# Kernel tuning notes

Hardware: AMD Instinct MI355X
Metric: run time of the kernel (lower is better)

Reference implementation:

```python
import jax, jax.numpy as jnp
import numpy as np

B, T, F, H = 64, 1024, 160, 1024


def setup_inputs() -> dict:
    key = jax.random.key(0)
    ks = jax.random.split(key, 18)
    s = lambda k, shape, scale=0.05: (jax.random.normal(k, shape, jnp.float32) * scale)
    inp = {
        "x": jax.random.normal(ks[0], (B, T, F), jnp.float32),
        # encoder GRU layer 0 (input F -> hidden H), PyTorch gate order r,z,n
        "Wih0": s(ks[1], (3 * H, F)), "Whh0": s(ks[2], (3 * H, H)),
        "bih0": s(ks[3], (3 * H,)), "bhh0": s(ks[4], (3 * H,)),
        # encoder GRU layer 1 (input H -> hidden H)
        "Wih1": s(ks[5], (3 * H, H)), "Whh1": s(ks[6], (3 * H, H)),
        "bih1": s(ks[7], (3 * H,)), "bhh1": s(ks[8], (3 * H,)),
        # fc: (n_enc_layers*H) -> H
        "fcW": s(ks[9], (H, 2 * H)), "fcb": jnp.zeros((H,), jnp.float32),
        # decoder GRUCell (input F -> hidden H)
        "dWih": s(ks[10], (3 * H, F)), "dWhh": s(ks[11], (3 * H, H)),
        "dbih": s(ks[12], (3 * H,)), "dbhh": s(ks[13], (3 * H,)),
        # dec_proj: H -> F
        "pW": s(ks[14], (F, H)), "pb": jnp.zeros((F,), jnp.float32),
    }
    return inp


def gru_step(h, xt, Wih, Whh, bih, bhh):
    # PyTorch GRU/GRUCell math, gate order (r, z, n)
    gi = xt @ Wih.T + bih          # [B, 3H]
    gh = h @ Whh.T + bhh           # [B, 3H]
    ir, iz, inn = jnp.split(gi, 3, axis=-1)
    hr, hz, hn = jnp.split(gh, 3, axis=-1)
    r = jax.nn.sigmoid(ir + hr)
    z = jax.nn.sigmoid(iz + hz)
    n = jnp.tanh(inn + r * hn)
    return (1.0 - z) * n + z * h


def reference(x, Wih0, Whh0, bih0, bhh0, Wih1, Whh1, bih1, bhh1,
              fcW, fcb, dWih, dWhh, dbih, dbhh, pW, pb):
    Bx, Tx = x.shape[0], x.shape[1]
    xs = jnp.swapaxes(x, 0, 1)  # [T, B, F]

    def run_layer(seq, Wih, Whh, bih, bhh):
        h0 = jnp.zeros((Bx, Whh.shape[1]), x.dtype)
        def step(h, xt):
            h = gru_step(h, xt, Wih, Whh, bih, bhh)
            return h, h
        hT, hs = jax.lax.scan(step, h0, seq)
        return hT, hs

    # 2-layer encoder GRU (dropout disabled: eval-mode / deterministic reference)
    h1, hs0 = run_layer(xs, Wih0, Whh0, bih0, bhh0)
    h2, _ = run_layer(hs0, Wih1, Whh1, bih1, bhh1)

    # h_n permute+view -> concat(layer0, layer1) along features
    h = jnp.tanh(jnp.concatenate([h1, h2], axis=-1) @ fcW.T + fcb)  # [B, H]

    i0 = jnp.zeros((Bx, pW.shape[0]), x.dtype)
    def dec_step(carry, _):
        hd, i = carry
        hd = gru_step(hd, i, dWih, dWhh, dbih, dbhh)
        i = hd @ pW.T + pb
        return (hd, i), i
    _, outs = jax.lax.scan(dec_step, (h, i0), None, length=Tx)  # [T, B, F]
    return jnp.swapaxes(outs, 0, 1)  # [B, T, F]
```

## Files before the change

### kernel.cpp

```cpp
#include <hip/hip_runtime.h>
#include <math.h>

#define NWG 256
#define NTH 512
#define MASTER 255

typedef _Float16 f16;
typedef __attribute__((ext_vector_type(8))) _Float16 h8;
typedef __attribute__((ext_vector_type(4))) float f4;

namespace {
constexpr int T_ = 1024, F_ = 160, H_ = 1024;
constexpr float SC = 2048.f;
constexpr float INV = 1.f / 2048.f;

constexpr int ESLOTH = 512 * 64 * 8;
constexpr int DSLOTH = 256 * 64 * 8;
constexpr int ELO = 256;
constexpr int DLO = 128;

constexpr size_t WS_BAR  = 0;
constexpr size_t WS_CVEC = 32896;
constexpr size_t WS_WDEC = WS_CVEC + 12288;
constexpr size_t WS_ENCA = WS_WDEC + (size_t)4 * H_ * H_ * 4;
constexpr size_t WS_DECA = WS_ENCA + (size_t)2 * ESLOTH * 2;
constexpr size_t WS_STRM = WS_DECA + (size_t)2 * DSLOTH * 2;

constexpr int DBUF_B = 135168;
constexpr int TBUF_B = DBUF_B + 17408;
constexpr int ZP_B   = TBUF_B + 2048;
constexpr int LDS_B  = ZP_B + 64;
}

__device__ __forceinline__ f4 MF(h8 a, h8 b, f4 c) {
  return __builtin_amdgcn_mfma_f32_16x16x32_f16(a, b, c, 0, 0, 0);
}

__device__ __forceinline__ void fsplit(float v, f16& hi, f16& lo) {
  const float hf = (fabsf(v) >= 6.103515625e-05f) ? (float)(f16)v : 0.f;
  hi = (f16)hf;
  lo = (f16)((v - hf) * SC);
}

__device__ __forceinline__ void gbar(unsigned* bar, int wg, unsigned& phase) {
  __syncthreads();
  ++phase;
  const int tid = threadIdx.x;
  unsigned* gen = bar + 8192;
  if (wg == MASTER) {
    if (tid == 0)
      __hip_atomic_store(&bar[MASTER * 32], phase, __ATOMIC_RELEASE, __HIP_MEMORY_SCOPE_AGENT);
    if (tid < 256) {
      while (__hip_atomic_load(&bar[tid * 32], __ATOMIC_RELAXED, __HIP_MEMORY_SCOPE_AGENT) < phase)
        __builtin_amdgcn_s_sleep(1);
    }
    __syncthreads();
    if (tid == 0) {
      __hip_atomic_store(gen, phase, __ATOMIC_RELEASE, __HIP_MEMORY_SCOPE_AGENT);
      (void)__hip_atomic_load(gen, __ATOMIC_ACQUIRE, __HIP_MEMORY_SCOPE_AGENT);
    }
  } else {
    if (tid == 0) {
      __hip_atomic_store(&bar[wg * 32], phase, __ATOMIC_RELEASE, __HIP_MEMORY_SCOPE_AGENT);
      while (__hip_atomic_load(gen, __ATOMIC_RELAXED, __HIP_MEMORY_SCOPE_AGENT) < phase)
        __builtin_amdgcn_s_sleep(1);
      (void)__hip_atomic_load(gen, __ATOMIC_ACQUIRE, __HIP_MEMORY_SCOPE_AGENT);
    }
  }
  __syncthreads();
}

__device__ void stageEnc(f16* __restrict__ whi, f16* __restrict__ wlo,
                         const float* __restrict__ Wx, const float* __restrict__ Wh,
                         int KX, int XOo, int KO, int u0, int tid) {
  for (int task = tid; task < KO * 24; task += NTH) {
    const int oct = task / 24;
    const int sl = task - oct * 24;
    const int g = (sl < 16) ? (sl >> 3) : 2;
    const int u = u0 + (sl & 7);
    const float* src = (oct < XOo)
        ? (Wx + (size_t)(g * H_ + u) * KX + (size_t)oct * 8)
        : (Wh + (size_t)(g * H_ + u) * H_ + (size_t)(oct - XOo) * 8);
    const float4 a = *(const float4*)src;
    const float4 b = *(const float4*)(src + 4);
    const float v[8] = {a.x, a.y, a.z, a.w, b.x, b.y, b.z, b.w};
    h8 hv, lv;
#pragma unroll
    for (int e = 0; e < 8; ++e) { f16 hh, ll; fsplit(v[e], hh, ll); hv[e] = hh; lv[e] = ll; }
    *(h8*)(whi + ((size_t)oct * 25 + sl) * 8) = hv;
    if (wlo) *(h8*)(wlo + ((size_t)oct * 25 + sl) * 8) = lv;
  }
}

__device__ void stageDec(f16* __restrict__ whi, f16* __restrict__ wlo,
                         const float* __restrict__ wdec, const float* __restrict__ dWhh,
                         int u0, int tid, bool t1set) {
  for (int task = tid; task < 128 * 32; task += NTH) {
    const int oct = task >> 5, sl = task & 31;
    const int g = sl >> 3;
    const int u = u0 + (sl & 7);
    float v[8];
    if (t1set) {
      if (g == 2) {
#pragma unroll
        for (int e = 0; e < 8; ++e) v[e] = 0.f;
      } else {
        const float* s = dWhh + (size_t)((g == 3 ? 2 : g) * H_ + u) * H_ + (size_t)oct * 8;
        const float4 a = *(const float4*)s, b = *(const float4*)(s + 4);
        v[0]=a.x; v[1]=a.y; v[2]=a.z; v[3]=a.w; v[4]=b.x; v[5]=b.y; v[6]=b.z; v[7]=b.w;
      }
    } else {
      const float* s = wdec + (size_t)(g * H_ + u) * H_ + (size_t)oct * 8;
      const float4 a = *(const float4*)s, b = *(const float4*)(s + 4);
      v[0]=a.x; v[1]=a.y; v[2]=a.z; v[3]=a.w; v[4]=b.x; v[5]=b.y; v[6]=b.z; v[7]=b.w;
    }
    h8 hv, lv;
#pragma unroll
    for (int e = 0; e < 8; ++e) { f16 hh, ll; fsplit(v[e], hh, ll); hv[e] = hh; lv[e] = ll; }
    *(h8*)(whi + ((size_t)oct * 33 + sl) * 8) = hv;
    *(h8*)(wlo + ((size_t)oct * 33 + sl) * 8) = lv;
  }
}

__device__ void stageProj(f16* __restrict__ whi, f16* __restrict__ wlo,
                          const float* __restrict__ pW, int f0, int tid) {
  for (int task = tid; task < 128 * 16; task += NTH) {
    const int oct = task >> 4, sl = task & 15;
    const float* s = pW + (size_t)(f0 + sl) * H_ + (size_t)oct * 8;
    const float4 a = *(const float4*)s, b = *(const float4*)(s + 4);
    const float v[8] = {a.x, a.y, a.z, a.w, b.x, b.y, b.z, b.w};
    h8 hv, lv;
#pragma unroll
    for (int e = 0; e < 8; ++e) { f16 hh, ll; fsplit(v[e], hh, ll); hv[e] = hh; lv[e] = ll; }
    *(h8*)(whi + ((size_t)oct * 17 + sl) * 8) = hv;
    *(h8*)(wlo + ((size_t)oct * 17 + sl) * 8) = lv;
  }
}

template<int NT, bool NSPLIT, int ROWH, bool STRM>
__device__ __forceinline__ void gmm(f4* Dh, f4* Dc,
    const f16* __restrict__ Ab, int aoctBase, int loOct,
    const f16* __restrict__ whi, const f16* __restrict__ wlo,
    const f16* __restrict__ strm,
    int ktn, int octBase, int XO, int ls, int lq, int lane,
    const f16* __restrict__ zp) {
  auto LD = [&](int kk, h8& ah, h8& al, h8& bh0, h8& bl0, h8& bh1, h8& bl1) {
    const int aoct = aoctBase + kk * 4 + lq;
    ah = *(const h8*)(Ab + (size_t)aoct * 512);
    al = *(const h8*)(Ab + (size_t)(aoct + loOct) * 512);
    const int oct = octBase + kk * 4 + lq;
    bh0 = *(const h8*)(whi + ((size_t)oct * ROWH + ls) * 8);
    if constexpr (STRM) bl0 = *(const h8*)(strm + ((size_t)(kk * 2) * 64 + lane) * 8);
    else bl0 = *(const h8*)(wlo + ((size_t)oct * ROWH + ls) * 8);
    if constexpr (NT == 2) {
      bool act = true; int psl;
      if constexpr (NSPLIT) { act = (ls < 8) ? (oct < XO) : (oct >= XO); psl = 16 + (ls & 7); }
      else { psl = 16 + ls; }
      bh1 = *(const h8*)(act ? (whi + ((size_t)oct * ROWH + psl) * 8) : zp);
      if constexpr (STRM) bl1 = *(const h8*)(strm + ((size_t)(kk * 2 + 1) * 64 + lane) * 8);
      else bl1 = *(const h8*)(act ? (wlo + ((size_t)oct * ROWH + psl) * 8) : zp);
    }
  };
  h8 ah, al, bh0, bl0, bh1, bl1;
  LD(0, ah, al, bh0, bl0, bh1, bl1);
  for (int kk = 0; kk < ktn; ++kk) {
    h8 ah2, al2, bh02, bl02, bh12, bl12;
    const int nk = (kk + 1 < ktn) ? (kk + 1) : kk;
    LD(nk, ah2, al2, bh02, bl02, bh12, bl12);
    Dh[0] = MF(ah, bh0, Dh[0]);
    Dc[0] = MF(al, bh0, Dc[0]);
    Dc[0] = MF(ah, bl0, Dc[0]);
    if constexpr (NT == 2) {
      Dh[1] = MF(ah, bh1, Dh[1]);
      Dc[1] = MF(al, bh1, Dc[1]);
      Dc[1] = MF(ah, bl1, Dc[1]);
    }
    ah = ah2; al = al2; bh0 = bh02; bl0 = bl02;
    if constexpr (NT == 2) { bh1 = bh12; bl1 = bl12; }
  }
}

__device__ __forceinline__ void gmm_x(f4* Dh, f4* Dc, const float* __restrict__ xp,
    const f16* __restrict__ whi, const f16* __restrict__ wlo,
    int ls, int lq, const f16* __restrict__ zp) {
#pragma unroll
  for (int kk = 0; kk < 5; ++kk) {
    const float4 a = *(const float4*)(xp + kk * 32);
    const float4 b = *(const float4*)(xp + kk * 32 + 4);
    const float v[8] = {a.x, a.y, a.z, a.w, b.x, b.y, b.z, b.w};
    h8 ah, al;
#pragma unroll
    for (int e = 0; e < 8; ++e) { f16 hh, ll; fsplit(v[e], hh, ll); ah[e] = hh; al[e] = ll; }
    const int oct = kk * 4 + lq;
    {
      const h8 bh2 = *(const h8*)(whi + ((size_t)oct * 25 + ls) * 8);
      const h8 bl2 = *(const h8*)(wlo + ((size_t)oct * 25 + ls) * 8);
      Dh[0] = MF(ah, bh2, Dh[0]);
      Dc[0] = MF(al, bh2, Dc[0]);
      Dc[0] = MF(ah, bl2, Dc[0]);
    }
    {
      const bool act = (ls < 8);
      const int psl = 16 + (ls & 7);
      const h8 bh2 = *(const h8*)(act ? (whi + ((size_t)oct * 25 + psl) * 8) : zp);
      const h8 bl2 = *(const h8*)(act ? (wlo + ((size_t)oct * 25 + psl) * 8) : zp);
      Dh[1] = MF(ah, bh2, Dh[1]);
      Dc[1] = MF(al, bh2, Dc[1]);
      Dc[1] = MF(ah, bl2, Dc[1]);
    }
  }
}

__global__ void build_c_kernel(const float* __restrict__ dWih, const float* __restrict__ dbih,
                               const float* __restrict__ pb, float* __restrict__ cvec) {
  const int r = blockIdx.x * 256 + threadIdx.x;
  if (r >= 3 * H_) return;
  float a = dbih[r];
  for (int f = 0; f < F_; ++f) a += dWih[(size_t)r * F_ + f] * pb[f];
  cvec[r] = a;
}

__global__ void build_wdec_kernel(const float* __restrict__ dWih, const float* __restrict__ dWhh,
                                  const float* __restrict__ pW, float* __restrict__ wdec) {
  const int idx = blockIdx.x * 256 + threadIdx.x;
  if (idx >= 3 * H_ * 128) return;
  const int row = idx >> 7;
  const int oct = idx & 127;
  float v[8] = {0, 0, 0, 0, 0, 0, 0, 0};
  const float* wr = dWih + (size_t)row * F_;
  for (int f = 0; f < F_; ++f) {
    const float w = wr[f];
    const float4 p0 = *(const float4*)(pW + (size_t)f * H_ + oct * 8);
    const float4 p1 = *(const float4*)(pW + (size_t)f * H_ + oct * 8 + 4);
    v[0] += w * p0.x; v[1] += w * p0.y; v[2] += w * p0.z; v[3] += w * p0.w;
    v[4] += w * p1.x; v[5] += w * p1.y; v[6] += w * p1.z; v[7] += w * p1.w;
  }
  if ((row >> 10) < 2) {
    const float* hr = dWhh + (size_t)row * H_ + oct * 8;
#pragma unroll
    for (int e = 0; e < 8; ++e) v[e] += hr[e];
  }
  float* o = wdec + (size_t)row * H_ + oct * 8;
#pragma unroll
  for (int e = 0; e < 8; ++e) o[e] = v[e];
}
__global__ void build_wdec_nh(const float* __restrict__ dWhh, float* __restrict__ wdec) {
  const int idx = blockIdx.x * 256 + threadIdx.x;
  if (idx >= H_ * H_) return;
  wdec[(size_t)3 * H_ * H_ + idx] = dWhh[(size_t)2 * H_ * H_ + idx];
}

__global__ void build_strm(const float* __restrict__ Wih1, const float* __restrict__ Whh1,
                           f16* __restrict__ strm) {
  const size_t idx = (size_t)blockIdx.x * 256 + threadIdx.x;
  const int j = (int)(idx & 7);
  const int lane = (int)((idx >> 3) & 63);
  const int nt = (int)((idx >> 9) & 1);
  const int kk = (int)((idx >> 10) & 31);
  const int kb = (int)((idx >> 15) & 1);
  const int wg = (int)(idx >> 16);
  const int c = lane & 15, lq = lane >> 4;
  const int oct = kb * 128 + kk * 4 + lq;
  const int k = oct * 8 + j;
  float v = 0.f;
  if (nt == 0) {
    const int row = (c >> 3) * H_ + wg * 8 + (c & 7);
    v = (oct < 128) ? Wih1[(size_t)row * H_ + k] : Whh1[(size_t)row * H_ + (k - 1024)];
  } else {
    const bool act = (c < 8) ? (oct < 128) : (oct >= 128);
    if (act) {
      const int row = 2 * H_ + wg * 8 + (c & 7);
      v = (oct < 128) ? Wih1[(size_t)row * H_ + k] : Whh1[(size_t)row * H_ + (k - 1024)];
    }
  }
  f16 hh, ll; fsplit(v, hh, ll);
  strm[idx] = ll;
}

__global__ void __launch_bounds__(NTH, 1) speech_ae_persistent(
    const float* __restrict__ x,
    const float* __restrict__ Wih0, const float* __restrict__ Whh0,
    const float* __restrict__ bih0, const float* __restrict__ bhh0,
    const float* __restrict__ Wih1, const float* __restrict__ Whh1,
    const float* __restrict__ bih1, const float* __restrict__ bhh1,
    const float* __restrict__ fcW, const float* __restrict__ fcb,
    const float* __restrict__ dbih, const float* __restrict__ dbhh,
    const float* __restrict__ pW, const float* __restrict__ pb,
    const float* __restrict__ dWhh,
    float* __restrict__ out, void* ws) {
  extern __shared__ char ldsb[];
  f16* wh = (f16*)ldsb;
  float* dbuf = (float*)(ldsb + DBUF_B);
  float* tbuf = (float*)(ldsb + TBUF_B);
  f16* zp = (f16*)(ldsb + ZP_B);

  char* wsb = (char*)ws;
  unsigned* bar = (unsigned*)(wsb + WS_BAR);
  const float* cvec = (const float*)(wsb + WS_CVEC);
  const float* wdec = (const float*)(wsb + WS_WDEC);
  f16* encA = (f16*)(wsb + WS_ENCA);
  f16* decA = (f16*)(wsb + WS_DECA);
  const f16* strm = (const f16*)(wsb + WS_STRM);

  const int tid = threadIdx.x, wg = blockIdx.x;
  const int lane = tid & 63, wv = tid >> 6;
  const int ls = lane & 15, lq = lane >> 4;
  const int m0 = (wv & 3) * 16, kb = wv >> 2;
  const int mb = m0 + ls;
  const bool isL1 = (wg < 128);
  unsigned phase = 0;
  const f16* strmW = strm + (size_t)(wg * 2 + kb) * 32768;

  const float* bi = isL1 ? bih1 : bih0;
  const float* bh_ = isL1 ? bhh1 : bhh0;
  const int eru = (isL1 ? wg * 8 : (wg - 128) * 8) + wv;
  const float ebr = bi[eru] + bh_[eru];
  const float ebz = bi[H_ + eru] + bh_[H_ + eru];
  const float ebni = bi[2 * H_ + eru];
  const float ebnh = bh_[2 * H_ + eru];
  float hreg = 0.f;

  float b1r = 0, b1z = 0, b1ni = 0, b1nh = 0, bfr = 0, bfz = 0, bfni = 0, bfnh = 0, hdreg = 0.f;
  if (wg < 128) {
    const int rw = wg * 8 + wv;
    b1r = dbih[rw] + dbhh[rw];
    b1z = dbih[H_ + rw] + dbhh[H_ + rw];
    b1ni = dbih[2 * H_ + rw];
    b1nh = dbhh[2 * H_ + rw];
    bfr = cvec[rw] + dbhh[rw];
    bfz = cvec[H_ + rw] + dbhh[H_ + rw];
    bfni = cvec[2 * H_ + rw];
    bfnh = dbhh[2 * H_ + rw];
  }
  const int f0 = (wg - 128) * 16;
  float pbr[4] = {0, 0, 0, 0};
  if (wg >= 128 && wg < 138 && tid < 256) {
    const int fq = tid & 3;
#pragma unroll
    for (int e = 0; e < 4; ++e) pbr[e] = pb[f0 + fq * 4 + e];
  }

  if (isL1) stageEnc(wh, nullptr, Wih1, Whh1, H_, 128, 256, wg * 8, tid);
  else stageEnc(wh, wh + 29600, Wih0, Whh0, F_, 20, 148, (wg - 128) * 8, tid);
  if (tid < 16) zp[tid] = (f16)0.f;
  __syncthreads();

  for (int s = 0; s <= T_; ++s) {
    const bool active = isL1 ? (s >= 1) : (s < T_);
    if (active) {
      const int t = isL1 ? (s - 1) : s;
      f4 Dh[2] = {{0.f,0.f,0.f,0.f},{0.f,0.f,0.f,0.f}};
      f4 Dc[2] = {{0.f,0.f,0.f,0.f},{0.f,0.f,0.f,0.f}};
      if (isL1) {
        if (kb == 0) {
          const f16* Ab = encA + (size_t)(t & 1) * ESLOTH + (size_t)mb * 8;
          gmm<2, true, 25, true>(Dh, Dc, Ab, 0, ELO, wh, nullptr, strmW, 32, 0, 128, ls, lq, lane, zp);
        } else if (t >= 1) {
          const f16* Ab = encA + (size_t)((t - 1) & 1) * ESLOTH + (size_t)mb * 8;
          gmm<2, true, 25, true>(Dh, Dc, Ab, 128, ELO, wh, nullptr, strmW, 32, 128, 128, ls, lq, lane, zp);
        }
      } else {
        if (kb == 0) {
          const float* xp = x + ((size_t)mb * T_ + t) * F_ + lq * 8;
          gmm_x(Dh, Dc, xp, wh, wh + 29600, ls, lq, zp);
          if (t >= 1) {
            const f16* Ab = encA + (size_t)((t - 1) & 1) * ESLOTH + (size_t)mb * 8;
            gmm<2, true, 25, false>(Dh, Dc, Ab, 0, ELO, wh, wh + 29600, nullptr, 14, 20, 20, ls, lq, lane, zp);
          }
        } else if (t >= 1) {
          const f16* Ab = encA + (size_t)((t - 1) & 1) * ESLOTH + (size_t)mb * 8;
          gmm<2, true, 25, false>(Dh, Dc, Ab, 56, ELO, wh, wh + 29600, nullptr, 18, 76, 20, ls, lq, lane, zp);
        }
      }
      *(f4*)(dbuf + kb * 2176 + ls * 68 + m0 + lq * 4) = Dh[0] + Dc[0] * INV;
      *(f4*)(dbuf + kb * 2176 + (16 + ls) * 68 + m0 + lq * 4) = Dh[1] + Dc[1] * INV;
      __syncthreads();
      const int b = lane;
      const float gr  = dbuf[wv * 68 + b]        + dbuf[2176 + wv * 68 + b]        + ebr;
      const float gz  = dbuf[(8 + wv) * 68 + b]  + dbuf[2176 + (8 + wv) * 68 + b]  + ebz;
      const float gni = dbuf[(16 + wv) * 68 + b] + dbuf[2176 + (16 + wv) * 68 + b] + ebni;
      const float gnh = dbuf[(24 + wv) * 68 + b] + dbuf[2176 + (24 + wv) * 68 + b] + ebnh;
      const float rg = 1.f / (1.f + expf(-gr));
      const float zg = 1.f / (1.f + expf(-gz));
      const float ng = tanhf(gni + rg * gnh);
      const float hn = (1.f - zg) * ng + zg * hreg;
      hreg = hn;
      tbuf[wv * 64 + b] = hn;
      __syncthreads();
      if (tid < 64) {
        const int oct = isL1 ? (128 + wg) : (wg - 128);
        f16* dst = encA + (size_t)(t & 1) * ESLOTH + ((size_t)oct * 64 + tid) * 8;
        h8 hv, lv;
#pragma unroll
        for (int e = 0; e < 8; ++e) { f16 hh, ll; fsplit(tbuf[e * 64 + tid], hh, ll); hv[e] = hh; lv[e] = ll; }
        *(h8*)dst = hv;
        *(h8*)(dst + (size_t)ELO * 512) = lv;
      }
    }
    gbar(bar, wg, phase);
  }

  if (wg < 128) {
    const int u0f = wg * 8;
    const int b = lane;
    float acc[8] = {0, 0, 0, 0, 0, 0, 0, 0};
    for (int ko = wv * 32; ko < wv * 32 + 32; ++ko) {
      const f16* hp = encA + ESLOTH + ((size_t)ko * 64 + b) * 8;
      const h8 hiv = *(const h8*)hp;
      const h8 lov = *(const h8*)(hp + (size_t)ELO * 512);
      float hv[8];
#pragma unroll
      for (int e = 0; e < 8; ++e) hv[e] = (float)hiv[e] + (float)lov[e] * INV;
#pragma unroll
      for (int u = 0; u < 8; ++u) {
        const float* wr = fcW + (size_t)(u0f + u) * 2048 + (size_t)ko * 8;
        const float4 wa = *(const float4*)wr, wb = *(const float4*)(wr + 4);
        acc[u] += hv[0] * wa.x + hv[1] * wa.y + hv[2] * wa.z + hv[3] * wa.w
                + hv[4] * wb.x + hv[5] * wb.y + hv[6] * wb.z + hv[7] * wb.w;
      }
    }
    __syncthreads();
#pragma unroll
    for (int u = 0; u < 8; ++u) dbuf[(u * 8 + wv) * 68 + b] = acc[u];
    __syncthreads();
    float sum = fcb[u0f + wv];
#pragma unroll
    for (int g = 0; g < 8; ++g) sum += dbuf[(wv * 8 + g) * 68 + lane];
    tbuf[wv * 64 + lane] = tanhf(sum);
    __syncthreads();
    if (tid < 64) {
      f16* dst = decA + ((size_t)wg * 64 + tid) * 8;
      h8 hv, lv;
#pragma unroll
      for (int e = 0; e < 8; ++e) { f16 hh, ll; fsplit(tbuf[e * 64 + tid], hh, ll); hv[e] = hh; lv[e] = ll; }
      *(h8*)dst = hv;
      *(h8*)(dst + (size_t)DLO * 512) = lv;
    }
  }
  if (wg < 128) stageDec(wh, wh + 33792, nullptr, dWhh, wg * 8, tid, true);
  else if (wg < 138) stageProj(wh, wh + 17408, pW, f0, tid);
  gbar(bar, wg, phase);

  auto dec_step = [&](int t, bool first) {
    f4 Dh[2] = {{0.f,0.f,0.f,0.f},{0.f,0.f,0.f,0.f}};
    f4 Dc[2] = {{0.f,0.f,0.f,0.f},{0.f,0.f,0.f,0.f}};
    const f16* Ab = decA + (size_t)((t - 1) & 1) * DSLOTH + (size_t)mb * 8;
    gmm<2, false, 33, false>(Dh, Dc, Ab, kb * 64, DLO, wh, wh + 33792, nullptr, 16, kb * 64, 0, ls, lq, lane, zp);
    *(f4*)(dbuf + kb * 2176 + ls * 68 + m0 + lq * 4) = Dh[0] + Dc[0] * INV;
    *(f4*)(dbuf + kb * 2176 + (16 + ls) * 68 + m0 + lq * 4) = Dh[1] + Dc[1] * INV;
    __syncthreads();
    const int b = lane;
    const float hprev = first ? tbuf[wv * 64 + b] : hdreg;
    const float gr  = dbuf[wv * 68 + b]        + dbuf[2176 + wv * 68 + b]        + (first ? b1r : bfr);
    const float gz  = dbuf[(8 + wv) * 68 + b]  + dbuf[2176 + (8 + wv) * 68 + b]  + (first ? b1z : bfz);
    const float gni = dbuf[(16 + wv) * 68 + b] + dbuf[2176 + (16 + wv) * 68 + b] + (first ? b1ni : bfni);
    const float gnh = dbuf[(24 + wv) * 68 + b] + dbuf[2176 + (24 + wv) * 68 + b] + (first ? b1nh : bfnh);
    const float rg = 1.f / (1.f + expf(-gr));
    const float zg = 1.f / (1.f + expf(-gz));
    const float ng = tanhf(gni + rg * gnh);
    const float hn = (1.f - zg) * ng + zg * hprev;
    hdreg = hn;
    tbuf[wv * 64 + b] = hn;
    __syncthreads();
    if (tid < 64) {
      f16* dst = decA + (size_t)(t & 1) * DSLOTH + ((size_t)wg * 64 + tid) * 8;
      h8 hv, lv;
#pragma unroll
      for (int e = 0; e < 8; ++e) { f16 hh, ll; fsplit(tbuf[e * 64 + tid], hh, ll); hv[e] = hh; lv[e] = ll; }
      *(h8*)dst = hv;
      *(h8*)(dst + (size_t)DLO * 512) = lv;
    }
  };

  auto proj = [&](int t2) {
    f4 Dh[1] = {{0.f,0.f,0.f,0.f}};
    f4 Dc[1] = {{0.f,0.f,0.f,0.f}};
    const f16* Ab = decA + (size_t)((t2 - 1) & 1) * DSLOTH + (size_t)mb * 8;
    gmm<1, false, 17, false>(Dh, Dc, Ab, kb * 64, DLO, wh, wh + 17408, nullptr, 16, kb * 64, 0, ls, lq, lane, zp);
    *(f4*)(dbuf + kb * 2176 + ls * 68 + m0 + lq * 4) = Dh[0] + Dc[0] * INV;
    __syncthreads();
    if (tid < 256) {
      const int b2 = tid >> 2, fq = tid & 3;
      float4 o;
      o.x = dbuf[(fq * 4 + 0) * 68 + b2] + dbuf[2176 + (fq * 4 + 0) * 68 + b2] + pbr[0];
      o.y = dbuf[(fq * 4 + 1) * 68 + b2] + dbuf[2176 + (fq * 4 + 1) * 68 + b2] + pbr[1];
      o.z = dbuf[(fq * 4 + 2) * 68 + b2] + dbuf[2176 + (fq * 4 + 2) * 68 + b2] + pbr[2];
      o.w = dbuf[(fq * 4 + 3) * 68 + b2] + dbuf[2176 + (fq * 4 + 3) * 68 + b2] + pbr[3];
      *(float4*)(out + (size_t)b2 * (T_ * F_) + (size_t)(t2 - 2) * F_ + f0 + fq * 4) = o;
    }
  };

  if (wg < 128) dec_step(1, true);
  gbar(bar, wg, phase);
  if (wg < 128) {
    stageDec(wh, wh + 33792, wdec, nullptr, wg * 8, tid, false);
    __syncthreads();
  }

  for (int t2 = 2; t2 <= T_ + 1; ++t2) {
    if (wg < 128) {
      if (t2 <= T_) dec_step(t2, false);
    } else if (wg < 138) {
      proj(t2);
    }
    gbar(bar, wg, phase);
  }
}

extern "C" void kernel_launch(void* const* d_in, const int* in_sizes, int n_in,
                              void* d_out, int out_size, void* d_ws, size_t ws_size,
                              hipStream_t stream) {
  (void)in_sizes; (void)n_in; (void)out_size; (void)ws_size;
  const float* x    = (const float*)d_in[0];
  const float* Wih0 = (const float*)d_in[1];
  const float* Whh0 = (const float*)d_in[2];
  const float* bih0 = (const float*)d_in[3];
  const float* bhh0 = (const float*)d_in[4];
  const float* Wih1 = (const float*)d_in[5];
  const float* Whh1 = (const float*)d_in[6];
  const float* bih1 = (const float*)d_in[7];
  const float* bhh1 = (const float*)d_in[8];
  const float* fcW  = (const float*)d_in[9];
  const float* fcb  = (const float*)d_in[10];
  const float* dWih = (const float*)d_in[11];
  const float* dWhh = (const float*)d_in[12];
  const float* dbih = (const float*)d_in[13];
  const float* dbhh = (const float*)d_in[14];
  const float* pW   = (const float*)d_in[15];
  const float* pb   = (const float*)d_in[16];
  float* out = (float*)d_out;
  char* wsb = (char*)d_ws;

  hipFuncSetAttribute((const void*)speech_ae_persistent,
                      hipFuncAttributeMaxDynamicSharedMemorySize, LDS_B);
  hipMemsetAsync(d_ws, 0, 32896, stream);
  build_c_kernel<<<(3 * H_ + 255) / 256, 256, 0, stream>>>(dWih, dbih, pb, (float*)(wsb + WS_CVEC));
  build_wdec_kernel<<<(3 * H_ * 128 + 255) / 256, 256, 0, stream>>>(dWih, dWhh, pW, (float*)(wsb + WS_WDEC));
  build_wdec_nh<<<(H_ * H_ + 255) / 256, 256, 0, stream>>>(dWhh, (float*)(wsb + WS_WDEC));
  build_strm<<<32768, 256, 0, stream>>>(Wih1, Whh1, (f16*)(wsb + WS_STRM));
  speech_ae_persistent<<<NWG, NTH, LDS_B, stream>>>(
      x, Wih0, Whh0, bih0, bhh0, Wih1, Whh1, bih1, bhh1, fcW, fcb,
      dbih, dbhh, pW, pb, dWhh, out, d_ws);
}
```

Measured before the change: 36.26 ms.

## Stage shared activations into per-XCD local copies with XCD-local barriers

```diff
diff --git a/kernel.cpp b/kernel.cpp
--- a/kernel.cpp
+++ b/kernel.cpp
@@ -20,11 +20,13 @@
 constexpr int DLO = 128;
 
 constexpr size_t WS_BAR  = 0;
-constexpr size_t WS_CVEC = 32896;
+constexpr size_t WS_CVEC = 49152;
 constexpr size_t WS_WDEC = WS_CVEC + 12288;
 constexpr size_t WS_ENCA = WS_WDEC + (size_t)4 * H_ * H_ * 4;
 constexpr size_t WS_DECA = WS_ENCA + (size_t)2 * ESLOTH * 2;
 constexpr size_t WS_STRM = WS_DECA + (size_t)2 * DSLOTH * 2;
+constexpr size_t WS_STG  = WS_STRM + (size_t)8388608 * 2;
+constexpr size_t WS_NEED = WS_STG + (size_t)8 * 524288;
 
 constexpr int DBUF_B = 135168;
 constexpr int TBUF_B = DBUF_B + 17408;
@@ -68,6 +70,51 @@
     }
   }
   __syncthreads();
+}
+
+__device__ __forceinline__ void lbar(unsigned* bar, unsigned& lphase, int myx, int slot) {
+  __syncthreads();
+  ++lphase;
+  const int tid = threadIdx.x;
+  unsigned* xgen = bar + 10752 + myx * 32;
+  if (slot == 0) {
+    if (tid >= 1 && tid < 32) {
+      while (__hip_atomic_load(&bar[8704 + myx * 256 + tid * 8], __ATOMIC_RELAXED, __HIP_MEMORY_SCOPE_AGENT) < lphase)
+        __builtin_amdgcn_s_sleep(1);
+    }
+    __syncthreads();
+    if (tid == 0) {
+      __hip_atomic_store(xgen, lphase, __ATOMIC_RELEASE, __HIP_MEMORY_SCOPE_AGENT);
+      (void)__hip_atomic_load(xgen, __ATOMIC_ACQUIRE, __HIP_MEMORY_SCOPE_AGENT);
+    }
+  } else {
+    if (tid == 0) {
+      __hip_atomic_store(&bar[8704 + myx * 256 + slot * 8], lphase, __ATOMIC_RELEASE, __HIP_MEMORY_SCOPE_AGENT);
+      while (__hip_atomic_load(xgen, __ATOMIC_RELAXED, __HIP_MEMORY_SCOPE_AGENT) < lphase)
+        __builtin_amdgcn_s_sleep(1);
+      (void)__hip_atomic_load(xgen, __ATOMIC_ACQUIRE, __HIP_MEMORY_SCOPE_AGENT);
+    }
+  }
+  __syncthreads();
+}
+
+__device__ __forceinline__ void enc_copy(const f16* encA, f16* stgX, int s, int slot, int tid) {
+  const int oct = slot * 16 + (tid >> 5);
+  const int l32 = tid & 31;
+  const size_t par = (size_t)((((oct & 128) ? s : (s - 1)) & 1)) * ESLOTH;
+  const f16* src = encA + par + (size_t)oct * 512 + l32 * 16;
+  f16* dst = stgX + (size_t)oct * 512 + l32 * 16;
+  const h8 a = *(const h8*)src;
+  const h8 b = *(const h8*)(src + 8);
+  *(h8*)dst = a;
+  *(h8*)(dst + 8) = b;
+}
+__device__ __forceinline__ void dec_copy(const f16* decA, f16* stgX, int t, int slot, int tid) {
+  const int oct = slot * 8 + (tid >> 6);
+  const int l64 = tid & 63;
+  const f16* src = decA + (size_t)((t - 1) & 1) * DSLOTH + (size_t)oct * 512 + l64 * 8;
+  f16* dst = stgX + (size_t)oct * 512 + l64 * 8;
+  *(h8*)dst = *(const h8*)src;
 }
 
 __device__ void stageEnc(f16* __restrict__ whi, f16* __restrict__ wlo,
@@ -287,8 +334,9 @@
     const float* __restrict__ dbih, const float* __restrict__ dbhh,
     const float* __restrict__ pW, const float* __restrict__ pb,
     const float* __restrict__ dWhh,
-    float* __restrict__ out, void* ws) {
+    float* __restrict__ out, void* ws, int stgok) {
   extern __shared__ char ldsb[];
+  __shared__ int bc[3];
   f16* wh = (f16*)ldsb;
   float* dbuf = (float*)(ldsb + DBUF_B);
   float* tbuf = (float*)(ldsb + TBUF_B);
@@ -308,8 +356,26 @@
   const int m0 = (wv & 3) * 16, kb = wv >> 2;
   const int mb = m0 + ls;
   const bool isL1 = (wg < 128);
-  unsigned phase = 0;
+  unsigned phase = 0, lphase = 0;
   const f16* strmW = strm + (size_t)(wg * 2 + kb) * 32768;
+
+  if (tid == 0) {
+    const unsigned myx = __builtin_amdgcn_s_getreg((31 << 11) | (0 << 6) | 20) & 15u;
+    const unsigned slot = __hip_atomic_fetch_add(&bar[11264 + myx * 16], 1u,
+                              __ATOMIC_RELAXED, __HIP_MEMORY_SCOPE_AGENT);
+    __hip_atomic_fetch_add(&bar[11520], 1u, __ATOMIC_ACQ_REL, __HIP_MEMORY_SCOPE_AGENT);
+    while (__hip_atomic_load(&bar[11520], __ATOMIC_RELAXED, __HIP_MEMORY_SCOPE_AGENT) < (unsigned)NWG)
+      __builtin_amdgcn_s_sleep(8);
+    (void)__hip_atomic_load(&bar[11520], __ATOMIC_ACQUIRE, __HIP_MEMORY_SCOPE_AGENT);
+    int okv = 1, groups = 0; unsigned total = 0;
+    for (int xx = 0; xx < 16; ++xx) {
+      const unsigned c = __hip_atomic_load(&bar[11264 + xx * 16], __ATOMIC_RELAXED, __HIP_MEMORY_SCOPE_AGENT);
+      if (c != 0) { ++groups; if (c != 32u) okv = 0; }
+      total += c;
+    }
+    if (groups != 8 || total != (unsigned)NWG || slot >= 32u) okv = 0;
+    bc[0] = (int)myx; bc[1] = (int)slot; bc[2] = okv && stgok;
+  }
 
   const float* bi = isL1 ? bih1 : bih0;
   const float* bh_ = isL1 ? bhh1 : bhh0;
@@ -345,7 +411,11 @@
   if (tid < 16) zp[tid] = (f16)0.f;
   __syncthreads();
 
+  const int myx = bc[0], slotId = bc[1], okf = bc[2];
+  f16* stgX = (f16*)(wsb + WS_STG) + (size_t)myx * 262144;
+
   for (int s = 0; s <= T_; ++s) {
+    if (okf && s >= 1) { enc_copy(encA, stgX, s, slotId, tid); lbar(bar, lphase, myx, slotId); }
     const bool active = isL1 ? (s >= 1) : (s < T_);
     if (active) {
       const int t = isL1 ? (s - 1) : s;
@@ -353,22 +423,23 @@
       f4 Dc[2] = {{0.f,0.f,0.f,0.f},{0.f,0.f,0.f,0.f}};
       if (isL1) {
         if (kb == 0) {
-          const f16* Ab = encA + (size_t)(t & 1) * ESLOTH + (size_t)mb * 8;
+          const f16* Ab = okf ? (stgX + (size_t)mb * 8)
+                              : (encA + (size_t)(t & 1) * ESLOTH + (size_t)mb * 8);
           gmm<2, true, 25, true>(Dh, Dc, Ab, 0, ELO, wh, nullptr, strmW, 32, 0, 128, ls, lq, lane, zp);
         } else if (t >= 1) {
-          const f16* Ab = encA + (size_t)((t - 1) & 1) * ESLOTH + (size_t)mb * 8;
+          const f16* Ab = okf ? (stgX + (size_t)mb * 8)
+                              : (encA + (size_t)((t - 1) & 1) * ESLOTH + (size_t)mb * 8);
           gmm<2, true, 25, true>(Dh, Dc, Ab, 128, ELO, wh, nullptr, strmW, 32, 128, 128, ls, lq, lane, zp);
         }
       } else {
+        const f16* Ab = okf ? (stgX + (size_t)mb * 8)
+                            : (encA + (size_t)((s - 1) & 1) * ESLOTH + (size_t)mb * 8);
         if (kb == 0) {
           const float* xp = x + ((size_t)mb * T_ + t) * F_ + lq * 8;
           gmm_x(Dh, Dc, xp, wh, wh + 29600, ls, lq, zp);
-          if (t >= 1) {
-            const f16* Ab = encA + (size_t)((t - 1) & 1) * ESLOTH + (size_t)mb * 8;
+          if (t >= 1)
             gmm<2, true, 25, false>(Dh, Dc, Ab, 0, ELO, wh, wh + 29600, nullptr, 14, 20, 20, ls, lq, lane, zp);
-          }
         } else if (t >= 1) {
-          const f16* Ab = encA + (size_t)((t - 1) & 1) * ESLOTH + (size_t)mb * 8;
           gmm<2, true, 25, false>(Dh, Dc, Ab, 56, ELO, wh, wh + 29600, nullptr, 18, 76, 20, ls, lq, lane, zp);
         }
       }
@@ -444,7 +515,8 @@
   auto dec_step = [&](int t, bool first) {
     f4 Dh[2] = {{0.f,0.f,0.f,0.f},{0.f,0.f,0.f,0.f}};
     f4 Dc[2] = {{0.f,0.f,0.f,0.f},{0.f,0.f,0.f,0.f}};
-    const f16* Ab = decA + (size_t)((t - 1) & 1) * DSLOTH + (size_t)mb * 8;
+    const f16* Ab = okf ? (stgX + (size_t)mb * 8)
+                        : (decA + (size_t)((t - 1) & 1) * DSLOTH + (size_t)mb * 8);
     gmm<2, false, 33, false>(Dh, Dc, Ab, kb * 64, DLO, wh, wh + 33792, nullptr, 16, kb * 64, 0, ls, lq, lane, zp);
     *(f4*)(dbuf + kb * 2176 + ls * 68 + m0 + lq * 4) = Dh[0] + Dc[0] * INV;
     *(f4*)(dbuf + kb * 2176 + (16 + ls) * 68 + m0 + lq * 4) = Dh[1] + Dc[1] * INV;
@@ -475,7 +547,8 @@
   auto proj = [&](int t2) {
     f4 Dh[1] = {{0.f,0.f,0.f,0.f}};
     f4 Dc[1] = {{0.f,0.f,0.f,0.f}};
-    const f16* Ab = decA + (size_t)((t2 - 1) & 1) * DSLOTH + (size_t)mb * 8;
+    const f16* Ab = okf ? (stgX + (size_t)mb * 8)
+                        : (decA + (size_t)((t2 - 1) & 1) * DSLOTH + (size_t)mb * 8);
     gmm<1, false, 17, false>(Dh, Dc, Ab, kb * 64, DLO, wh, wh + 17408, nullptr, 16, kb * 64, 0, ls, lq, lane, zp);
     *(f4*)(dbuf + kb * 2176 + ls * 68 + m0 + lq * 4) = Dh[0] + Dc[0] * INV;
     __syncthreads();
@@ -490,6 +563,7 @@
     }
   };
 
+  if (okf) { dec_copy(decA, stgX, 1, slotId, tid); lbar(bar, lphase, myx, slotId); }
   if (wg < 128) dec_step(1, true);
   gbar(bar, wg, phase);
   if (wg < 128) {
@@ -498,6 +572,7 @@
   }
 
   for (int t2 = 2; t2 <= T_ + 1; ++t2) {
+    if (okf) { dec_copy(decA, stgX, t2, slotId, tid); lbar(bar, lphase, myx, slotId); }
     if (wg < 128) {
       if (t2 <= T_) dec_step(t2, false);
     } else if (wg < 138) {
@@ -510,7 +585,7 @@
 extern "C" void kernel_launch(void* const* d_in, const int* in_sizes, int n_in,
                               void* d_out, int out_size, void* d_ws, size_t ws_size,
                               hipStream_t stream) {
-  (void)in_sizes; (void)n_in; (void)out_size; (void)ws_size;
+  (void)in_sizes; (void)n_in; (void)out_size;
   const float* x    = (const float*)d_in[0];
   const float* Wih0 = (const float*)d_in[1];
   const float* Whh0 = (const float*)d_in[2];
@@ -531,14 +606,16 @@
   float* out = (float*)d_out;
   char* wsb = (char*)d_ws;
 
+  const int stgok = (ws_size >= WS_NEED) ? 1 : 0;
+
   hipFuncSetAttribute((const void*)speech_ae_persistent,
                       hipFuncAttributeMaxDynamicSharedMemorySize, LDS_B);
-  hipMemsetAsync(d_ws, 0, 32896, stream);
+  hipMemsetAsync(d_ws, 0, 49152, stream);
   build_c_kernel<<<(3 * H_ + 255) / 256, 256, 0, stream>>>(dWih, dbih, pb, (float*)(wsb + WS_CVEC));
   build_wdec_kernel<<<(3 * H_ * 128 + 255) / 256, 256, 0, stream>>>(dWih, dWhh, pW, (float*)(wsb + WS_WDEC));
   build_wdec_nh<<<(H_ * H_ + 255) / 256, 256, 0, stream>>>(dWhh, (float*)(wsb + WS_WDEC));
   build_strm<<<32768, 256, 0, stream>>>(Wih1, Whh1, (f16*)(wsb + WS_STRM));
   speech_ae_persistent<<<NWG, NTH, LDS_B, stream>>>(
       x, Wih0, Whh0, bih0, bhh0, Wih1, Whh1, bih1, bhh1, fcW, fcb,
-      dbih, dbhh, pW, pb, dWhh, out, d_ws);
-}
+      dbih, dbhh, pW, pb, dWhh, out, d_ws, stgok);
+}
```

New measurement: 73.29 ms. 102% more time.

## Retile per-step GEMMs to 2x2 M-tiles per wave with 4-way K split

Applied to the files above, without the earlier changes.

```diff
diff --git a/kernel.cpp b/kernel.cpp
--- a/kernel.cpp
+++ b/kernel.cpp
@@ -138,16 +138,21 @@
 }
 
 template<int NT, bool NSPLIT, int ROWH, bool STRM>
-__device__ __forceinline__ void gmm(f4* Dh, f4* Dc,
+__device__ __forceinline__ void gmm(f4 Dh[2][2], f4 Dc[2][2],
     const f16* __restrict__ Ab, int aoctBase, int loOct,
     const f16* __restrict__ whi, const f16* __restrict__ wlo,
     const f16* __restrict__ strm,
     int ktn, int octBase, int XO, int ls, int lq, int lane,
     const f16* __restrict__ zp) {
-  auto LD = [&](int kk, h8& ah, h8& al, h8& bh0, h8& bl0, h8& bh1, h8& bl1) {
+  auto LD = [&](int kk, h8& a0, h8& l0, h8& a1, h8& l1,
+                h8& bh0, h8& bl0, h8& bh1, h8& bl1) {
     const int aoct = aoctBase + kk * 4 + lq;
-    ah = *(const h8*)(Ab + (size_t)aoct * 512);
-    al = *(const h8*)(Ab + (size_t)(aoct + loOct) * 512);
+    const f16* ap = Ab + (size_t)aoct * 512;
+    const f16* lp = Ab + (size_t)(aoct + loOct) * 512;
+    a0 = *(const h8*)ap;
+    a1 = *(const h8*)(ap + 128);
+    l0 = *(const h8*)lp;
+    l1 = *(const h8*)(lp + 128);
     const int oct = octBase + kk * 4 + lq;
     bh0 = *(const h8*)(whi + ((size_t)oct * ROWH + ls) * 8);
     if constexpr (STRM) bl0 = *(const h8*)(strm + ((size_t)(kk * 2) * 64 + lane) * 8);
@@ -161,52 +166,69 @@
       else bl1 = *(const h8*)(act ? (wlo + ((size_t)oct * ROWH + psl) * 8) : zp);
     }
   };
-  h8 ah, al, bh0, bl0, bh1, bl1;
-  LD(0, ah, al, bh0, bl0, bh1, bl1);
+  h8 a0, l0, a1, l1, bh0, bl0, bh1, bl1;
+  LD(0, a0, l0, a1, l1, bh0, bl0, bh1, bl1);
   for (int kk = 0; kk < ktn; ++kk) {
-    h8 ah2, al2, bh02, bl02, bh12, bl12;
+    h8 a0n, l0n, a1n, l1n, bh0n, bl0n, bh1n, bl1n;
     const int nk = (kk + 1 < ktn) ? (kk + 1) : kk;
-    LD(nk, ah2, al2, bh02, bl02, bh12, bl12);
-    Dh[0] = MF(ah, bh0, Dh[0]);
-    Dc[0] = MF(al, bh0, Dc[0]);
-    Dc[0] = MF(ah, bl0, Dc[0]);
+    LD(nk, a0n, l0n, a1n, l1n, bh0n, bl0n, bh1n, bl1n);
+    Dh[0][0] = MF(a0, bh0, Dh[0][0]);
+    Dc[0][0] = MF(l0, bh0, Dc[0][0]);
+    Dc[0][0] = MF(a0, bl0, Dc[0][0]);
+    Dh[1][0] = MF(a1, bh0, Dh[1][0]);
+    Dc[1][0] = MF(l1, bh0, Dc[1][0]);
+    Dc[1][0] = MF(a1, bl0, Dc[1][0]);
     if constexpr (NT == 2) {
-      Dh[1] = MF(ah, bh1, Dh[1]);
-      Dc[1] = MF(al, bh1, Dc[1]);
-      Dc[1] = MF(ah, bl1, Dc[1]);
-    }
-    ah = ah2; al = al2; bh0 = bh02; bl0 = bl02;
-    if constexpr (NT == 2) { bh1 = bh12; bl1 = bl12; }
-  }
-}
-
-__device__ __forceinline__ void gmm_x(f4* Dh, f4* Dc, const float* __restrict__ xp,
+      Dh[0][1] = MF(a0, bh1, Dh[0][1]);
+      Dc[0][1] = MF(l0, bh1, Dc[0][1]);
+      Dc[0][1] = MF(a0, bl1, Dc[0][1]);
+      Dh[1][1] = MF(a1, bh1, Dh[1][1]);
+      Dc[1][1] = MF(l1, bh1, Dc[1][1]);
+      Dc[1][1] = MF(a1, bl1, Dc[1][1]);
+    }
+    a0 = a0n; l0 = l0n; a1 = a1n; l1 = l1n; bh0 = bh0n; bl0 = bl0n;
+    if constexpr (NT == 2) { bh1 = bh1n; bl1 = bl1n; }
+  }
+}
+
+__device__ __forceinline__ void gmm_x2(f4 Dh[2][2], f4 Dc[2][2],
+    const float* __restrict__ xp0, const float* __restrict__ xp1,
     const f16* __restrict__ whi, const f16* __restrict__ wlo,
     int ls, int lq, const f16* __restrict__ zp) {
 #pragma unroll
   for (int kk = 0; kk < 5; ++kk) {
-    const float4 a = *(const float4*)(xp + kk * 32);
-    const float4 b = *(const float4*)(xp + kk * 32 + 4);
-    const float v[8] = {a.x, a.y, a.z, a.w, b.x, b.y, b.z, b.w};
-    h8 ah, al;
-#pragma unroll
-    for (int e = 0; e < 8; ++e) { f16 hh, ll; fsplit(v[e], hh, ll); ah[e] = hh; al[e] = ll; }
+    h8 am[2], lm[2];
+#pragma unroll
+    for (int mt = 0; mt < 2; ++mt) {
+      const float* xp = mt ? xp1 : xp0;
+      const float4 a = *(const float4*)(xp + kk * 32);
+      const float4 b = *(const float4*)(xp + kk * 32 + 4);
+      const float v[8] = {a.x, a.y, a.z, a.w, b.x, b.y, b.z, b.w};
+#pragma unroll
+      for (int e = 0; e < 8; ++e) { f16 hh, ll; fsplit(v[e], hh, ll); am[mt][e] = hh; lm[mt][e] = ll; }
+    }
     const int oct = kk * 4 + lq;
     {
       const h8 bh2 = *(const h8*)(whi + ((size_t)oct * 25 + ls) * 8);
       const h8 bl2 = *(const h8*)(wlo + ((size_t)oct * 25 + ls) * 8);
-      Dh[0] = MF(ah, bh2, Dh[0]);
-      Dc[0] = MF(al, bh2, Dc[0]);
-      Dc[0] = MF(ah, bl2, Dc[0]);
+#pragma unroll
+      for (int mt = 0; mt < 2; ++mt) {
+        Dh[mt][0] = MF(am[mt], bh2, Dh[mt][0]);
+        Dc[mt][0] = MF(lm[mt], bh2, Dc[mt][0]);
+        Dc[mt][0] = MF(am[mt], bl2, Dc[mt][0]);
+      }
     }
     {
       const bool act = (ls < 8);
       const int psl = 16 + (ls & 7);
       const h8 bh2 = *(const h8*)(act ? (whi + ((size_t)oct * 25 + psl) * 8) : zp);
       const h8 bl2 = *(const h8*)(act ? (wlo + ((size_t)oct * 25 + psl) * 8) : zp);
-      Dh[1] = MF(ah, bh2, Dh[1]);
-      Dc[1] = MF(al, bh2, Dc[1]);
-      Dc[1] = MF(ah, bl2, Dc[1]);
+#pragma unroll
+      for (int mt = 0; mt < 2; ++mt) {
+        Dh[mt][1] = MF(am[mt], bh2, Dh[mt][1]);
+        Dc[mt][1] = MF(lm[mt], bh2, Dc[mt][1]);
+        Dc[mt][1] = MF(am[mt], bl2, Dc[mt][1]);
+      }
     }
   }
 }
@@ -305,11 +327,12 @@
   const int tid = threadIdx.x, wg = blockIdx.x;
   const int lane = tid & 63, wv = tid >> 6;
   const int ls = lane & 15, lq = lane >> 4;
-  const int m0 = (wv & 3) * 16, kb = wv >> 2;
+  const int mg = wv & 1, kg = wv >> 1;
+  const int m0 = mg * 32;
   const int mb = m0 + ls;
   const bool isL1 = (wg < 128);
   unsigned phase = 0;
-  const f16* strmW = strm + (size_t)(wg * 2 + kb) * 32768;
+  const f16* strmQ = strm + (size_t)(wg * 2 + (kg >> 1)) * 32768 + (size_t)(kg & 1) * 16384;
 
   const float* bi = isL1 ? bih1 : bih0;
   const float* bh_ = isL1 ? bhh1 : bhh0;
@@ -345,36 +368,55 @@
   if (tid < 16) zp[tid] = (f16)0.f;
   __syncthreads();
 
+  auto combine = [&](f4 Dh[2][2], f4 Dc[2][2], int NTv) {
+    float* dp = dbuf + (kg & 1) * 2176;
+    const int c0 = m0 + lq * 4;
+    if (kg < 2) {
+      for (int mt = 0; mt < 2; ++mt)
+        for (int nt = 0; nt < NTv; ++nt)
+          *(f4*)(dp + (nt * 16 + ls) * 68 + c0 + mt * 16) = Dh[mt][nt] + Dc[mt][nt] * INV;
+    }
+    __syncthreads();
+    if (kg >= 2) {
+      for (int mt = 0; mt < 2; ++mt)
+        for (int nt = 0; nt < NTv; ++nt) {
+          f4* p = (f4*)(dp + (nt * 16 + ls) * 68 + c0 + mt * 16);
+          *p = *p + Dh[mt][nt] + Dc[mt][nt] * INV;
+        }
+    }
+    __syncthreads();
+  };
+
+  const f4 Z = {0.f, 0.f, 0.f, 0.f};
+
   for (int s = 0; s <= T_; ++s) {
     const bool active = isL1 ? (s >= 1) : (s < T_);
     if (active) {
       const int t = isL1 ? (s - 1) : s;
-      f4 Dh[2] = {{0.f,0.f,0.f,0.f},{0.f,0.f,0.f,0.f}};
-      f4 Dc[2] = {{0.f,0.f,0.f,0.f},{0.f,0.f,0.f,0.f}};
+      f4 Dh[2][2] = {{Z, Z}, {Z, Z}};
+      f4 Dc[2][2] = {{Z, Z}, {Z, Z}};
       if (isL1) {
-        if (kb == 0) {
+        if (kg < 2) {
           const f16* Ab = encA + (size_t)(t & 1) * ESLOTH + (size_t)mb * 8;
-          gmm<2, true, 25, true>(Dh, Dc, Ab, 0, ELO, wh, nullptr, strmW, 32, 0, 128, ls, lq, lane, zp);
+          gmm<2, true, 25, true>(Dh, Dc, Ab, kg * 64, ELO, wh, nullptr, strmQ, 16, kg * 64, 128, ls, lq, lane, zp);
         } else if (t >= 1) {
           const f16* Ab = encA + (size_t)((t - 1) & 1) * ESLOTH + (size_t)mb * 8;
-          gmm<2, true, 25, true>(Dh, Dc, Ab, 128, ELO, wh, nullptr, strmW, 32, 128, 128, ls, lq, lane, zp);
+          gmm<2, true, 25, true>(Dh, Dc, Ab, kg * 64, ELO, wh, nullptr, strmQ, 16, kg * 64, 128, ls, lq, lane, zp);
         }
       } else {
-        if (kb == 0) {
-          const float* xp = x + ((size_t)mb * T_ + t) * F_ + lq * 8;
-          gmm_x(Dh, Dc, xp, wh, wh + 29600, ls, lq, zp);
-          if (t >= 1) {
-            const f16* Ab = encA + (size_t)((t - 1) & 1) * ESLOTH + (size_t)mb * 8;
-            gmm<2, true, 25, false>(Dh, Dc, Ab, 0, ELO, wh, wh + 29600, nullptr, 14, 20, 20, ls, lq, lane, zp);
-          }
+        const f16* Ab = encA + (size_t)((s - 1) & 1) * ESLOTH + (size_t)mb * 8;
+        if (kg == 0) {
+          const float* xp0 = x + ((size_t)mb * T_ + t) * F_ + lq * 8;
+          const float* xp1 = xp0 + (size_t)16 * T_ * F_;
+          gmm_x2(Dh, Dc, xp0, xp1, wh, wh + 29600, ls, lq, zp);
+          if (t >= 1)
+            gmm<2, true, 25, false>(Dh, Dc, Ab, 0, ELO, wh, wh + 29600, nullptr, 5, 20, 20, ls, lq, lane, zp);
         } else if (t >= 1) {
-          const f16* Ab = encA + (size_t)((t - 1) & 1) * ESLOTH + (size_t)mb * 8;
-          gmm<2, true, 25, false>(Dh, Dc, Ab, 56, ELO, wh, wh + 29600, nullptr, 18, 76, 20, ls, lq, lane, zp);
+          const int ao = 20 + (kg - 1) * 36;
+          gmm<2, true, 25, false>(Dh, Dc, Ab, ao, ELO, wh, wh + 29600, nullptr, 9, 20 + ao, 20, ls, lq, lane, zp);
         }
       }
-      *(f4*)(dbuf + kb * 2176 + ls * 68 + m0 + lq * 4) = Dh[0] + Dc[0] * INV;
-      *(f4*)(dbuf + kb * 2176 + (16 + ls) * 68 + m0 + lq * 4) = Dh[1] + Dc[1] * INV;
-      __syncthreads();
+      combine(Dh, Dc, 2);
       const int b = lane;
       const float gr  = dbuf[wv * 68 + b]        + dbuf[2176 + wv * 68 + b]        + ebr;
       const float gz  = dbuf[(8 + wv) * 68 + b]  + dbuf[2176 + (8 + wv) * 68 + b]  + ebz;
@@ -442,13 +484,11 @@
   gbar(bar, wg, phase);
 
   auto dec_step = [&](int t, bool first) {
-    f4 Dh[2] = {{0.f,0.f,0.f,0.f},{0.f,0.f,0.f,0.f}};
-    f4 Dc[2] = {{0.f,0.f,0.f,0.f},{0.f,0.f,0.f,0.f}};
+    f4 Dh[2][2] = {{Z, Z}, {Z, Z}};
+    f4 Dc[2][2] = {{Z, Z}, {Z, Z}};
     const f16* Ab = decA + (size_t)((t - 1) & 1) * DSLOTH + (size_t)mb * 8;
-    gmm<2, false, 33, false>(Dh, Dc, Ab, kb * 64, DLO, wh, wh + 33792, nullptr, 16, kb * 64, 0, ls, lq, lane, zp);
-    *(f4*)(dbuf + kb * 2176 + ls * 68 + m0 + lq * 4) = Dh[0] + Dc[0] * INV;
-    *(f4*)(dbuf + kb * 2176 + (16 + ls) * 68 + m0 + lq * 4) = Dh[1] + Dc[1] * INV;
-    __syncthreads();
+    gmm<2, false, 33, false>(Dh, Dc, Ab, kg * 32, DLO, wh, wh + 33792, nullptr, 8, kg * 32, 0, ls, lq, lane, zp);
+    combine(Dh, Dc, 2);
     const int b = lane;
     const float hprev = first ? tbuf[wv * 64 + b] : hdreg;
     const float gr  = dbuf[wv * 68 + b]        + dbuf[2176 + wv * 68 + b]        + (first ? b1r : bfr);
@@ -473,12 +513,11 @@
   };
 
   auto proj = [&](int t2) {
-    f4 Dh[1] = {{0.f,0.f,0.f,0.f}};
-    f4 Dc[1] = {{0.f,0.f,0.f,0.f}};
+    f4 Dh[2][2] = {{Z, Z}, {Z, Z}};
+    f4 Dc[2][2] = {{Z, Z}, {Z, Z}};
     const f16* Ab = decA + (size_t)((t2 - 1) & 1) * DSLOTH + (size_t)mb * 8;
-    gmm<1, false, 17, false>(Dh, Dc, Ab, kb * 64, DLO, wh, wh + 17408, nullptr, 16, kb * 64, 0, ls, lq, lane, zp);
-    *(f4*)(dbuf + kb * 2176 + ls * 68 + m0 + lq * 4) = Dh[0] + Dc[0] * INV;
-    __syncthreads();
+    gmm<1, false, 17, false>(Dh, Dc, Ab, kg * 32, DLO, wh, wh + 17408, nullptr, 8, kg * 32, 0, ls, lq, lane, zp);
+    combine(Dh, Dc, 1);
     if (tid < 256) {
       const int b2 = tid >> 2, fq = tid & 3;
       float4 o;
```

Result: slower. 38.10 ms (+5.1%).
